# Optimization experiments

Measured on AMD Instinct MI355X. Metric: run time of the kernel, lower is better.

## Reference

```python
import jax, jax.numpy as jnp
import numpy as np

N = 50000
E = 800000
D_IN = 128
D_OUT = 128
BN_EPS = 1e-5


def setup_inputs() -> dict:
    key = jax.random.key(0)
    ks = jax.random.split(key, 9)
    feature = jax.random.normal(ks[0], (N, D_IN), dtype=jnp.float32)
    snorm_n = jax.random.uniform(ks[1], (N, 1), dtype=jnp.float32)
    edge_src = jax.random.randint(ks[2], (E,), 0, N, dtype=jnp.int32)
    edge_dst = jax.random.randint(ks[3], (E,), 0, N, dtype=jnp.int32)
    # Linear(in,out,bias=False) weights, applied as x @ W (W stored [in,out])
    s = 1.0 / np.sqrt(D_IN)
    W1 = jax.random.uniform(ks[4], (D_IN, D_OUT), jnp.float32, -s, s)
    W2 = jax.random.uniform(ks[5], (D_IN, D_OUT), jnp.float32, -s, s)
    W3 = jax.random.uniform(ks[6], (D_IN, D_OUT), jnp.float32, -s, s)
    bias = jnp.zeros((D_OUT,), jnp.float32)
    gamma = jnp.ones((D_OUT,), jnp.float32)
    beta = jnp.zeros((D_OUT,), jnp.float32)
    return {"feature": feature, "snorm_n": snorm_n, "W1": W1, "W2": W2,
            "W3": W3, "bias": bias, "gamma": gamma, "beta": beta,
            "edge_src": edge_src, "edge_dst": edge_dst}


def _mpconv(feat, norm, edge_src, edge_dst):
    # feat: [N, D]; norm: [N, 1] = clamp(in_deg,1)^-0.5
    h = feat * norm
    msg = h[edge_src]                                   # gather [E, D]
    agg = jax.ops.segment_sum(msg, edge_dst, num_segments=N)  # scatter-add
    return agg * norm


def reference(feature, snorm_n, W1, W2, W3, bias, gamma, beta,
              edge_src, edge_dst):
    # in-degree normalization (same graph for both MP passes)
    deg = jax.ops.segment_sum(jnp.ones_like(edge_dst, jnp.float32),
                              edge_dst, num_segments=N)
    norm = jnp.power(jnp.clip(deg, 1.0, None), -0.5)[:, None]  # [N,1]

    h_in = feature
    ax = _mpconv(feature, norm, edge_src, edge_dst)
    ax2 = _mpconv(ax, norm, edge_src, edge_dst)

    h = (feature @ W1) + ((-ax) @ W2) + ((2.0 * ax2 - feature) @ W3) + bias
    h = h * snorm_n  # graph_norm

    # BatchNorm1d over nodes (training-mode batch statistics, biased var)
    mean = jnp.mean(h, axis=0)
    var = jnp.mean(jnp.square(h - mean), axis=0)
    h = (h - mean) * jax.lax.rsqrt(var + BN_EPS) * gamma + beta

    h = jax.nn.relu(h)      # activation
    h = h_in + h            # residual (in_dim == out_dim)
    # dropout p=0.0 -> identity
    return h
```

## Files before the change

### kernel.cpp

```cpp
#include <hip/hip_runtime.h>
#include <hip/hip_bf16.h>

#define NN 50000
#define NE 800000
#define DD 128
#define BN_EPS 1e-5f
#define SCAN_G 98

typedef unsigned short ushort_t;
typedef unsigned int uint_t;
typedef __attribute__((ext_vector_type(8))) short short8v;
typedef __attribute__((ext_vector_type(4))) float f32x4;

__device__ __forceinline__ float b2f(ushort_t u) {
    union { uint_t i; float f; } v; v.i = ((uint_t)u) << 16; return v.f;
}
__device__ __forceinline__ ushort_t f2b(float f) {
    uint_t u = __float_as_uint(f);
    u += 0x7FFFu + ((u >> 16) & 1u);
    return (ushort_t)(u >> 16);
}
__device__ __forceinline__ void atomAdd(float* p, float v) { unsafeAtomicAdd(p, v); }

__global__ void epos_prep(const int* __restrict__ dst, int* __restrict__ cnt,
                          int* __restrict__ epos,
                          const float* __restrict__ feat, ushort_t* __restrict__ feat_bf) {
    int e = blockIdx.x * 256 + threadIdx.x;
    {
        const float4* fp = reinterpret_cast<const float4*>(feat);
        ushort4* op = reinterpret_cast<ushort4*>(feat_bf);
        int i = e << 1;
        float4 v0 = fp[i], v1 = fp[i + 1];
        ushort4 o0 = { f2b(v0.x), f2b(v0.y), f2b(v0.z), f2b(v0.w) };
        ushort4 o1 = { f2b(v1.x), f2b(v1.y), f2b(v1.z), f2b(v1.w) };
        op[i] = o0; op[i + 1] = o1;
    }
    epos[e] = atomicAdd(&cnt[dst[e]], 1);
}

__global__ __launch_bounds__(512) void scan_part(const int* __restrict__ deg,
                                                 int* __restrict__ part,
                                                 float* __restrict__ norm) {
    int i = blockIdx.x * 512 + threadIdx.x;
    int v = (i < NN) ? deg[i] : 0;
    if (i < NN) norm[i] = rsqrtf((float)max(v, 1));
    int s = v;
    #pragma unroll
    for (int k = 1; k < 64; k <<= 1) s += __shfl_xor(s, k);
    __shared__ int wsum[8];
    if ((threadIdx.x & 63) == 0) wsum[threadIdx.x >> 6] = s;
    __syncthreads();
    if (threadIdx.x == 0) {
        int t = 0;
        #pragma unroll
        for (int k = 0; k < 8; ++k) t += wsum[k];
        part[blockIdx.x] = t;
    }
}

__global__ __launch_bounds__(512) void scan_final(const int* __restrict__ deg,
                                                  const int* __restrict__ part,
                                                  int* __restrict__ off,
                                                  const float* __restrict__ W1,
                                                  const float* __restrict__ W2,
                                                  const float* __restrict__ W3,
                                                  ushort_t* __restrict__ wcT) {
    if (blockIdx.x >= SCAN_G) {
        int i = (blockIdx.x - SCAN_G) * 512 + threadIdx.x;
        int d = i / 384, k = i % 384;
        float v;
        if (k < 128)      v = W1[k * DD + d] - W3[k * DD + d];
        else if (k < 256) v = -W2[(k - 128) * DD + d];
        else              v = 2.0f * W3[(k - 256) * DD + d];
        wcT[i] = f2b(v);
        return;
    }
    __shared__ int wsum[8];
    __shared__ int sbase;
    int t = threadIdx.x;
    int lane = t & 63, wv = t >> 6;

    int p = (t < blockIdx.x && t < SCAN_G) ? part[t] : 0;
    #pragma unroll
    for (int s = 1; s < 64; s <<= 1) p += __shfl_xor(p, s);
    if (lane == 0) wsum[wv] = p;
    __syncthreads();
    if (t == 0) {
        int b = 0;
        #pragma unroll
        for (int k = 0; k < 8; ++k) b += wsum[k];
        sbase = b;
    }
    __syncthreads();

    int i = blockIdx.x * 512 + t;
    int v = (i < NN) ? deg[i] : 0;
    int incl = v;
    #pragma unroll
    for (int s = 1; s < 64; s <<= 1) {
        int u = __shfl_up(incl, s);
        if (lane >= s) incl += u;
    }
    __syncthreads();
    if (lane == 63) wsum[wv] = incl;
    __syncthreads();
    int woff = 0;
    for (int k = 0; k < wv; ++k) woff += wsum[k];
    int excl = sbase + woff + incl - v;
    if (i < NN) off[i] = excl;
    if (blockIdx.x == 0 && t == 0) off[NN] = NE;
}

__global__ void fill_kernel(const int* __restrict__ src, const int* __restrict__ dst,
                            const int* __restrict__ epos, const int* __restrict__ off,
                            const float* __restrict__ norm, int2* __restrict__ csr) {
    int e = blockIdx.x * 256 + threadIdx.x;
    if (e >= NE) return;
    int s = src[e];
    int p = off[dst[e]] + epos[e];
    csr[p] = make_int2(s, __float_as_int(norm[s]));
}

__global__ __launch_bounds__(256) void gather_bf(const ushort_t* __restrict__ x,
                                                 const float* __restrict__ norm,
                                                 const int* __restrict__ off,
                                                 const int2* __restrict__ csr,
                                                 ushort_t* __restrict__ out) {
    int g = (blockIdx.x << 4) | (threadIdx.x >> 4);
    int l4 = threadIdx.x & 15;
    int jb = off[g], je = off[g + 1];
    const uint4* xp = reinterpret_cast<const uint4*>(x);
    float a0 = 0.f, a1 = 0.f, a2 = 0.f, a3 = 0.f;
    float a4 = 0.f, a5 = 0.f, a6 = 0.f, a7 = 0.f;

#define ACC(cc, vv)                                                  \
    {                                                                \
        float n_ = __int_as_float(cc.y);                             \
        a0 = fmaf(n_, b2f((ushort_t)(vv.x)), a0);                    \
        a1 = fmaf(n_, b2f((ushort_t)(vv.x >> 16)), a1);              \
        a2 = fmaf(n_, b2f((ushort_t)(vv.y)), a2);                    \
        a3 = fmaf(n_, b2f((ushort_t)(vv.y >> 16)), a3);              \
        a4 = fmaf(n_, b2f((ushort_t)(vv.z)), a4);                    \
        a5 = fmaf(n_, b2f((ushort_t)(vv.z >> 16)), a5);              \
        a6 = fmaf(n_, b2f((ushort_t)(vv.w)), a6);                    \
        a7 = fmaf(n_, b2f((ushort_t)(vv.w >> 16)), a7);              \
    }

    int j = jb;
    for (; j + 4 <= je; j += 4) {
        int2 c0 = csr[j + 0];
        int2 c1 = csr[j + 1];
        int2 c2 = csr[j + 2];
        int2 c3 = csr[j + 3];
        uint4 v0 = xp[(size_t)c0.x * 16 + l4];
        uint4 v1 = xp[(size_t)c1.x * 16 + l4];
        uint4 v2 = xp[(size_t)c2.x * 16 + l4];
        uint4 v3 = xp[(size_t)c3.x * 16 + l4];
        ACC(c0, v0); ACC(c1, v1); ACC(c2, v2); ACC(c3, v3);
    }
    for (; j < je; ++j) {
        int2 c = csr[j];
        uint4 v = xp[(size_t)c.x * 16 + l4];
        ACC(c, v);
    }
#undef ACC

    float nd = norm[g];
    uint4 o;
    o.x = (uint_t)f2b(nd * a0) | ((uint_t)f2b(nd * a1) << 16);
    o.y = (uint_t)f2b(nd * a2) | ((uint_t)f2b(nd * a3) << 16);
    o.z = (uint_t)f2b(nd * a4) | ((uint_t)f2b(nd * a5) << 16);
    o.w = (uint_t)f2b(nd * a6) | ((uint_t)f2b(nd * a7) << 16);
    reinterpret_cast<uint4*>(out)[(size_t)g * 16 + l4] = o;
}

__global__ __launch_bounds__(256) void gemm_bn(
    const ushort_t* __restrict__ feat_bf, const ushort_t* __restrict__ ax_bf,
    const ushort_t* __restrict__ ax2_bf, const ushort_t* __restrict__ wcT,
    const float* __restrict__ bias, const float* __restrict__ snorm,
    ushort_t* __restrict__ t_out, float* __restrict__ gsums, float* __restrict__ gsq)
{
    __shared__ ushort_t As[128 * 128];
    __shared__ ushort_t Bs[128 * 128];
    int tid = threadIdx.x;
    int w = tid >> 6, lane = tid & 63;
    int row0 = blockIdx.x * 128;

    f32x4 acc[2][8] = {};

    #pragma unroll
    for (int kt = 0; kt < 3; ++kt) {
        const ushort_t* S = (kt == 0) ? feat_bf : (kt == 1) ? ax_bf : ax2_bf;
        __syncthreads();
        {
            int r = tid >> 1, hh = tid & 1;
            int grow = min(row0 + r, NN - 1);
            const char* gsrc = (const char*)(S + grow * DD);
            char* dbase = (char*)As + r * 256;
            int sw = (r & 7) << 4;
            #pragma unroll
            for (int c = 0; c < 8; ++c) {
                int cb = hh * 128 + c * 16;
                *(short8v*)(dbase + (cb ^ sw)) = *(const short8v*)(gsrc + cb);
            }
        }
        {
            int cidx = tid >> 1, hh = tid & 1;
            const char* gsrc = (const char*)(wcT + cidx * 384 + kt * 128);
            char* dbase = (char*)Bs + cidx * 256;
            int sw = (cidx & 7) << 4;
            #pragma unroll
            for (int c = 0; c < 8; ++c) {
                int cb = hh * 128 + c * 16;
                *(short8v*)(dbase + (cb ^ sw)) = *(const short8v*)(gsrc + cb);
            }
        }
        __syncthreads();
        int l15 = lane & 15;
        int r0a = w * 32 + l15;
        int r1a = r0a + 16;
        #pragma unroll
        for (int ks = 0; ks < 4; ++ks) {
            int kb = ks * 64 + ((lane >> 4) << 4);
            short8v a0 = *(const short8v*)((const char*)As + r0a * 256 + (kb ^ ((r0a & 7) << 4)));
            short8v a1 = *(const short8v*)((const char*)As + r1a * 256 + (kb ^ ((r1a & 7) << 4)));
            #pragma unroll
            for (int cf = 0; cf < 8; ++cf) {
                int col = cf * 16 + l15;
                short8v b = *(const short8v*)((const char*)Bs + col * 256 + (kb ^ ((col & 7) << 4)));
                acc[0][cf] = __builtin_amdgcn_mfma_f32_16x16x32_bf16(a0, b, acc[0][cf], 0, 0, 0);
                acc[1][cf] = __builtin_amdgcn_mfma_f32_16x16x32_bf16(a1, b, acc[1][cf], 0, 0, 0);
            }
        }
    }

    int q = lane >> 4, c0 = lane & 15;
    float s1[8], s2[8];
    #pragma unroll
    for (int cf = 0; cf < 8; ++cf) { s1[cf] = 0.f; s2[cf] = 0.f; }

    #pragma unroll
    for (int g = 0; g < 2; ++g) {
        int rbase = row0 + w * 32 + g * 16 + q * 4;
        float sn[4];
        #pragma unroll
        for (int i = 0; i < 4; ++i) sn[i] = (rbase + i < NN) ? snorm[rbase + i] : 0.f;
        #pragma unroll
        for (int cf = 0; cf < 8; ++cf) {
            int col = cf * 16 + c0;
            float bc = bias[col];
            #pragma unroll
            for (int i = 0; i < 4; ++i) {
                int row = rbase + i;
                if (row < NN) {
                    float t = (acc[g][cf][i] + bc) * sn[i];
                    t_out[row * DD + col] = f2b(t);
                    s1[cf] += t; s2[cf] += t * t;
                }
            }
        }
    }
    #pragma unroll
    for (int cf = 0; cf < 8; ++cf) {
        s1[cf] += __shfl_xor(s1[cf], 16); s1[cf] += __shfl_xor(s1[cf], 32);
        s2[cf] += __shfl_xor(s2[cf], 16); s2[cf] += __shfl_xor(s2[cf], 32);
    }
    if (q == 0) {
        int slot = (blockIdx.x & 31) * DD;
        #pragma unroll
        for (int cf = 0; cf < 8; ++cf) {
            atomAdd(&gsums[slot + cf * 16 + c0], s1[cf]);
            atomAdd(&gsq[slot + cf * 16 + c0], s2[cf]);
        }
    }
}

__global__ void bn_finalize(const float* __restrict__ gsums, const float* __restrict__ gsq,
                            const float* __restrict__ gamma,
                            const float* __restrict__ beta,
                            float* __restrict__ scale, float* __restrict__ shift) {
    int d = threadIdx.x;
    float s1 = 0.f, s2 = 0.f;
    for (int c = 0; c < 32; ++c) { s1 += gsums[c * DD + d]; s2 += gsq[c * DD + d]; }
    float mean = s1 / (float)NN;
    float var  = s2 / (float)NN - mean * mean;
    float sc = gamma[d] * rsqrtf(var + BN_EPS);
    scale[d] = sc;
    shift[d] = beta[d] - mean * sc;
}

__global__ void epilogue(const ushort_t* __restrict__ t, const ushort_t* __restrict__ featb,
                         const float* __restrict__ scale, const float* __restrict__ shift,
                         float* __restrict__ out) {
    int i = blockIdx.x * 256 + threadIdx.x;
    if (i >= NN * DD / 4) return;
    int d0 = (i << 2) & 127;
    ushort4 tv = reinterpret_cast<const ushort4*>(t)[i];
    ushort4 fv = reinterpret_cast<const ushort4*>(featb)[i];
    float4 o;
    o.x = b2f(fv.x) + fmaxf(b2f(tv.x) * scale[d0 + 0] + shift[d0 + 0], 0.f);
    o.y = b2f(fv.y) + fmaxf(b2f(tv.y) * scale[d0 + 1] + shift[d0 + 1], 0.f);
    o.z = b2f(fv.z) + fmaxf(b2f(tv.z) * scale[d0 + 2] + shift[d0 + 2], 0.f);
    o.w = b2f(fv.w) + fmaxf(b2f(tv.w) * scale[d0 + 3] + shift[d0 + 3], 0.f);
    reinterpret_cast<float4*>(out)[i] = o;
}

extern "C" void kernel_launch(void* const* d_in, const int* in_sizes, int n_in,
                              void* d_out, int out_size, void* d_ws, size_t ws_size,
                              hipStream_t stream) {
    const float* feat  = (const float*)d_in[0];
    const float* snorm = (const float*)d_in[1];
    const float* W1    = (const float*)d_in[2];
    const float* W2    = (const float*)d_in[3];
    const float* W3    = (const float*)d_in[4];
    const float* bias  = (const float*)d_in[5];
    const float* gamma = (const float*)d_in[6];
    const float* beta  = (const float*)d_in[7];
    const int* esrc = (const int*)d_in[8];
    const int* edst = (const int*)d_in[9];
    float* out = (float*)d_out;

    char* ws = (char*)d_ws;
    ushort_t* t_bf    = (ushort_t*)(ws);
    int*      epos    = (int*)     (ws);
    ushort_t* feat_bf = (ushort_t*)(ws + 12800000);
    ushort_t* ax_bf   = (ushort_t*)(ws + 25600000);
    ushort_t* ax2_bf  = (ushort_t*)(ws + 38400000);
    int2*     csr     = (int2*)    (ws + 51200000);
    float*    norm    = (float*)   (ws + 57600000);
    int*      cnt     = (int*)     (ws + 57800000);
    float*    gsums   = (float*)   (ws + 58000000);
    float*    gsq     = (float*)   (ws + 58016384);
    int*      off     = (int*)     (ws + 58032768);
    int*      part    = (int*)     (ws + 58232832);
    float*    scale   = (float*)   (ws + 58233856);
    float*    shift   = (float*)   (ws + 58234368);
    ushort_t* wcT     = (ushort_t*)(ws + 58234880);

    hipMemsetAsync(ws + 57800000, 0, 232768, stream);

    epos_prep  <<<3125, 256, 0, stream>>>(edst, cnt, epos, feat, feat_bf);
    scan_part  <<<SCAN_G, 512, 0, stream>>>(cnt, part, norm);
    scan_final <<<SCAN_G + 96, 512, 0, stream>>>(cnt, part, off, W1, W2, W3, wcT);
    fill_kernel<<<3125, 256, 0, stream>>>(esrc, edst, epos, off, norm, csr);

    gather_bf<<<3125, 256, 0, stream>>>(feat_bf, norm, off, csr, ax_bf);
    gather_bf<<<3125, 256, 0, stream>>>(ax_bf,   norm, off, csr, ax2_bf);

    gemm_bn<<<391, 256, 0, stream>>>(feat_bf, ax_bf, ax2_bf, wcT, bias, snorm,
                                     t_bf, gsums, gsq);
    bn_finalize<<<1, 128, 0, stream>>>(gsums, gsq, gamma, beta, scale, shift);
    epilogue   <<<6250, 256, 0, stream>>>(t_bf, feat_bf, scale, shift, out);
}
```

Before: 166.8 us.

## Replace global atomic degree counting with per-block LDS histograms and column scan

Counts destination-node degrees in per-block shared-memory histograms of packed 16-bit counters instead of global atomics, records each edge's local rank, then column-scans the per-block counts to get per-block prefixes and total degrees. The fill step combines the node offset, block prefix and local rank to place edges in CSR order. This also removes the memset by zeroing the stats buffers in-kernel, and folds the bf16 feature conversion into the 125-block counting kernel. The intent is to avoid contended global atomics, at the cost of a serial 125-step column scan, a large 100 KB LDS footprint per block with low occupancy, and only 125 blocks doing the feature conversion.

```diff
diff --git a/kernel.cpp b/kernel.cpp
--- a/kernel.cpp
+++ b/kernel.cpp
@@ -6,6 +6,9 @@
 #define DD 128
 #define BN_EPS 1e-5f
 #define SCAN_G 98
+#define NB 125
+#define CHUNK 6400
+#define NWRD 25000
 
 typedef unsigned short ushort_t;
 typedef unsigned int uint_t;
@@ -22,20 +25,54 @@
 }
 __device__ __forceinline__ void atomAdd(float* p, float v) { unsafeAtomicAdd(p, v); }
 
-__global__ void epos_prep(const int* __restrict__ dst, int* __restrict__ cnt,
-                          int* __restrict__ epos,
-                          const float* __restrict__ feat, ushort_t* __restrict__ feat_bf) {
-    int e = blockIdx.x * 256 + threadIdx.x;
+__global__ __launch_bounds__(256) void lds_count(const int* __restrict__ dst,
+                                                 int* __restrict__ cnt_block,
+                                                 ushort_t* __restrict__ rank16,
+                                                 const float* __restrict__ feat,
+                                                 ushort_t* __restrict__ feat_bf,
+                                                 float4* __restrict__ gz) {
+    __shared__ uint_t h[NWRD];
+    int b = blockIdx.x, t = threadIdx.x;
+    for (int i = t; i < NWRD; i += 256) h[i] = 0u;
     {
         const float4* fp = reinterpret_cast<const float4*>(feat);
         ushort4* op = reinterpret_cast<ushort4*>(feat_bf);
-        int i = e << 1;
-        float4 v0 = fp[i], v1 = fp[i + 1];
-        ushort4 o0 = { f2b(v0.x), f2b(v0.y), f2b(v0.z), f2b(v0.w) };
-        ushort4 o1 = { f2b(v1.x), f2b(v1.y), f2b(v1.z), f2b(v1.w) };
-        op[i] = o0; op[i + 1] = o1;
-    }
-    epos[e] = atomicAdd(&cnt[dst[e]], 1);
+        for (int i = b * 256 + t; i < 1600000; i += NB * 256) {
+            float4 v = fp[i];
+            ushort4 o = { f2b(v.x), f2b(v.y), f2b(v.z), f2b(v.w) };
+            op[i] = o;
+        }
+    }
+    if (b == 0) {
+        float4 z = make_float4(0.f, 0.f, 0.f, 0.f);
+        #pragma unroll
+        for (int k = 0; k < 8; ++k) gz[t + k * 256] = z;
+    }
+    __syncthreads();
+    int e0 = b * CHUNK;
+    #pragma unroll
+    for (int k = 0; k < CHUNK; k += 256) {
+        int e = e0 + k + t;
+        int d = dst[e];
+        int sh = (d & 1) << 4;
+        uint_t old = atomicAdd(&h[d >> 1], 1u << sh);
+        rank16[e] = (ushort_t)((old >> sh) & 0xFFFFu);
+    }
+    __syncthreads();
+    for (int i = t; i < NWRD; i += 256) cnt_block[b * NWRD + i] = (int)h[i];
+}
+
+__global__ __launch_bounds__(256) void col_scan(int* __restrict__ cnt_block,
+                                                int2* __restrict__ deg2) {
+    int w = blockIdx.x * 256 + threadIdx.x;
+    if (w >= NWRD) return;
+    uint_t run = 0;
+    for (int b = 0; b < NB; ++b) {
+        uint_t v = (uint_t)cnt_block[b * NWRD + w];
+        cnt_block[b * NWRD + w] = (int)run;
+        run += v;
+    }
+    deg2[w] = make_int2((int)(run & 0xFFFFu), (int)(run >> 16));
 }
 
 __global__ __launch_bounds__(512) void scan_part(const int* __restrict__ deg,
@@ -111,13 +148,18 @@
     if (blockIdx.x == 0 && t == 0) off[NN] = NE;
 }
 
-__global__ void fill_kernel(const int* __restrict__ src, const int* __restrict__ dst,
-                            const int* __restrict__ epos, const int* __restrict__ off,
-                            const float* __restrict__ norm, int2* __restrict__ csr) {
+__global__ void fill2(const int* __restrict__ src, const int* __restrict__ dst,
+                      const ushort_t* __restrict__ rank16,
+                      const int* __restrict__ cnt_block,
+                      const int* __restrict__ off,
+                      const float* __restrict__ norm, int2* __restrict__ csr) {
     int e = blockIdx.x * 256 + threadIdx.x;
     if (e >= NE) return;
-    int s = src[e];
-    int p = off[dst[e]] + epos[e];
+    int b = e / CHUNK;
+    int s = src[e], d = dst[e];
+    int sh = (d & 1) << 4;
+    uint_t pref = ((uint_t)cnt_block[b * NWRD + (d >> 1)] >> sh) & 0xFFFFu;
+    int p = off[d] + (int)pref + (int)rank16[e];
     csr[p] = make_int2(s, __float_as_int(norm[s]));
 }
 
@@ -322,13 +364,14 @@
 
     char* ws = (char*)d_ws;
     ushort_t* t_bf    = (ushort_t*)(ws);
-    int*      epos    = (int*)     (ws);
+    ushort_t* rank16  = (ushort_t*)(ws);
     ushort_t* feat_bf = (ushort_t*)(ws + 12800000);
     ushort_t* ax_bf   = (ushort_t*)(ws + 25600000);
+    int*      cnt_blk = (int*)     (ws + 25600000);
     ushort_t* ax2_bf  = (ushort_t*)(ws + 38400000);
     int2*     csr     = (int2*)    (ws + 51200000);
     float*    norm    = (float*)   (ws + 57600000);
-    int*      cnt     = (int*)     (ws + 57800000);
+    int*      deg     = (int*)     (ws + 57800000);
     float*    gsums   = (float*)   (ws + 58000000);
     float*    gsq     = (float*)   (ws + 58016384);
     int*      off     = (int*)     (ws + 58032768);
@@ -337,12 +380,12 @@
     float*    shift   = (float*)   (ws + 58234368);
     ushort_t* wcT     = (ushort_t*)(ws + 58234880);
 
-    hipMemsetAsync(ws + 57800000, 0, 232768, stream);
-
-    epos_prep  <<<3125, 256, 0, stream>>>(edst, cnt, epos, feat, feat_bf);
-    scan_part  <<<SCAN_G, 512, 0, stream>>>(cnt, part, norm);
-    scan_final <<<SCAN_G + 96, 512, 0, stream>>>(cnt, part, off, W1, W2, W3, wcT);
-    fill_kernel<<<3125, 256, 0, stream>>>(esrc, edst, epos, off, norm, csr);
+    lds_count <<<NB, 256, 0, stream>>>(edst, cnt_blk, rank16, feat, feat_bf,
+                                       (float4*)(ws + 58000000));
+    col_scan  <<<98, 256, 0, stream>>>(cnt_blk, (int2*)deg);
+    scan_part <<<SCAN_G, 512, 0, stream>>>(deg, part, norm);
+    scan_final<<<SCAN_G + 96, 512, 0, stream>>>(deg, part, off, W1, W2, W3, wcT);
+    fill2     <<<3125, 256, 0, stream>>>(esrc, edst, rank16, cnt_blk, off, norm, csr);
 
     gather_bf<<<3125, 256, 0, stream>>>(feat_bf, norm, off, csr, ax_bf);
     gather_bf<<<3125, 256, 0, stream>>>(ax_bf,   norm, off, csr, ax2_bf);
```

After: 168.3 us. No clear change (+0.9%).
